# Performance work log

Hardware: AMD Instinct MI355X
Metric: run time of the kernel (lower is better)

## Reference

```python
import jax, jax.numpy as jnp
import numpy as np

NUM_EXPERTS = 8
TOP_K = 2
HIDDEN = 1024
INTER = 4096
B, S = 4, 2048


def setup_inputs() -> dict:
    key = jax.random.key(0)
    ks = jax.random.split(key, 5)
    scale_h = 1.0 / np.sqrt(HIDDEN)
    scale_f = 1.0 / np.sqrt(INTER)
    return {
        "hidden_states": jax.random.normal(ks[0], (B, S, HIDDEN), dtype=jnp.float32),
        "router_w": jax.random.normal(ks[1], (HIDDEN, NUM_EXPERTS), dtype=jnp.float32) * scale_h,
        "gate_w": jax.random.normal(ks[2], (NUM_EXPERTS, HIDDEN, INTER), dtype=jnp.float32) * scale_h,
        "up_w": jax.random.normal(ks[3], (NUM_EXPERTS, HIDDEN, INTER), dtype=jnp.float32) * scale_h,
        "down_w": jax.random.normal(ks[4], (NUM_EXPERTS, INTER, HIDDEN), dtype=jnp.float32) * scale_f,
    }


def reference(hidden_states, router_w, gate_w, up_w, down_w):
    # hidden_states: [B, S, D]
    Bsz, Sl, D = hidden_states.shape
    E = gate_w.shape[0]

    router_logits = jnp.einsum("bsd,de->bse", hidden_states, router_w)
    router_probs = jax.nn.softmax(router_logits, axis=-1)          # [B,S,E]
    expert_weights, expert_indices = jax.lax.top_k(router_probs, TOP_K)  # [B,S,K]
    expert_weights = expert_weights / jnp.sum(expert_weights, axis=-1, keepdims=True)

    # load-balance loss: usage_e = count(idx==e)/num_tokens (sums to K)
    num_tokens = Bsz * Sl
    one_hot = jax.nn.one_hot(expert_indices, E, dtype=router_probs.dtype)  # [B,S,K,E]
    expert_usage = jnp.sum(one_hot, axis=(0, 1, 2)) / num_tokens           # [E]
    mean_routing_prob = jnp.mean(router_probs, axis=(0, 1))                # [E]
    load_balance_loss = jnp.sum(expert_usage * mean_routing_prob) * E

    # combine weight per token per expert: [B,S,E]
    combine_w = jnp.einsum("bsk,bske->bse", expert_weights, one_hot)

    output = jnp.zeros_like(hidden_states)
    for e in range(E):  # small fixed expert count
        gate = jax.nn.silu(jnp.einsum("bsd,df->bsf", hidden_states, gate_w[e]))
        up = jnp.einsum("bsd,df->bsf", hidden_states, up_w[e])
        expert_out = jnp.einsum("bsf,fd->bsd", gate * up, down_w[e])
        output = output + combine_w[..., e, None] * expert_out

    return output, load_balance_loss
```

## Files before the change

kernel.cpp:

```cpp
#include <hip/hip_runtime.h>
#include <stdint.h>

#define T_TOK 8192
#define D_HID 1024
#define F_INT 4096
#define NEXP 8
#define NT2 (T_TOK*2)
#define BMR 256
#define NTIL 72
#define CBANKS 64

typedef __attribute__((ext_vector_type(4))) float f32x4;
typedef __attribute__((ext_vector_type(8))) __bf16 bf16x8;
typedef unsigned short u16;

__device__ __forceinline__ unsigned short f2bf(float x) {
  unsigned int u = __float_as_uint(x);
  u = u + 0x7FFFu + ((u >> 16) & 1u);
  return (unsigned short)(u >> 16);
}
__device__ __forceinline__ float bf2f(u16 b) {
  return __uint_as_float(((unsigned)b) << 16);
}
__device__ __forceinline__ void gload_lds16(const void* g, void* l) {
  __builtin_amdgcn_global_load_lds(
      (const __attribute__((address_space(1))) unsigned int*)g,
      (__attribute__((address_space(3))) unsigned int*)l, 16, 0, 0);
}
__device__ __forceinline__ void wait_vm8() {
  asm volatile("s_waitcnt vmcnt(8)" ::: "memory");
  __builtin_amdgcn_sched_barrier(0);
}
__device__ __forceinline__ void wait_vm0() {
  asm volatile("s_waitcnt vmcnt(0)" ::: "memory");
  __builtin_amdgcn_sched_barrier(0);
}
__device__ __forceinline__ void wait_lgkm0() {
  asm volatile("s_waitcnt lgkmcnt(0)" ::: "memory");
  __builtin_amdgcn_sched_barrier(0);
}
__device__ __forceinline__ int tswz(int x) { return (x & 7) * 9 + (x >> 3); }

#define MFMA(a,b,c) __builtin_amdgcn_mfma_f32_16x16x32_bf16((a),(b),(c),0,0,0)

__global__ __launch_bounds__(256) void k_cvt(const float* __restrict__ in,
                                             u16* __restrict__ out, long n) {
  long i = ((long)blockIdx.x * 256 + threadIdx.x) * 4;
  long stride = (long)gridDim.x * 1024;
  for (; i < n; i += stride) {
    float4 v = *(const float4*)(in + i);
    union { u16 s[4]; uint2 v2; } o;
    o.s[0] = f2bf(v.x); o.s[1] = f2bf(v.y); o.s[2] = f2bf(v.z); o.s[3] = f2bf(v.w);
    *(uint2*)(out + i) = o.v2;
  }
}

__global__ __launch_bounds__(256) void k_cvt_t(const float* __restrict__ in,
                                               u16* __restrict__ out,
                                               int R, int C) {
  const size_t mat = (size_t)R * C;
  const float* ip = in + (size_t)blockIdx.z * mat;
  u16* op = out + (size_t)blockIdx.z * mat;
  int c0 = blockIdx.x * 64, r0 = blockIdx.y * 64;
  __shared__ u16 T[64][68];
  int t = threadIdx.x;
#pragma unroll
  for (int p = 0; p < 4; p++) {
    int r = p * 16 + (t >> 4);
    int c = (t & 15) * 4;
    float4 v = *(const float4*)(ip + (size_t)(r0 + r) * C + (c0 + c));
    union { u16 s[4]; uint2 q; } o;
    o.s[0] = f2bf(v.x); o.s[1] = f2bf(v.y); o.s[2] = f2bf(v.z); o.s[3] = f2bf(v.w);
    *(uint2*)&T[r][c] = o.q;
  }
  __syncthreads();
  int f = t >> 2, seg = (t & 3) * 16;
  __align__(16) u16 buf[16];
#pragma unroll
  for (int j = 0; j < 16; j++) buf[j] = T[seg + j][f];
  *(uint4*)(op + (size_t)(c0 + f) * R + r0 + seg) = *(uint4*)&buf[0];
  *(uint4*)(op + (size_t)(c0 + f) * R + r0 + seg + 8) = *(uint4*)&buf[8];
}

__global__ __launch_bounds__(256) void k_router(const float* __restrict__ h,
                                                const float* __restrict__ rw,
                                                int* __restrict__ cntB,
                                                float* __restrict__ psumB,
                                                int* __restrict__ topk_e,
                                                float* __restrict__ topk_w) {
  int t = blockIdx.x * 4 + (threadIdx.x >> 6);
  int l = threadIdx.x & 63;
  const float* hr = h + (size_t)t * D_HID;
  double acc[NEXP];
#pragma unroll
  for (int e = 0; e < NEXP; e++) acc[e] = 0.0;
  for (int i = l; i < D_HID; i += 64) {
    double x = (double)hr[i];
    const float4* r4 = (const float4*)(rw + (size_t)i * NEXP);
    float4 a = r4[0], b = r4[1];
    acc[0] += x * a.x; acc[1] += x * a.y; acc[2] += x * a.z; acc[3] += x * a.w;
    acc[4] += x * b.x; acc[5] += x * b.y; acc[6] += x * b.z; acc[7] += x * b.w;
  }
#pragma unroll
  for (int m = 32; m >= 1; m >>= 1) {
#pragma unroll
    for (int e = 0; e < NEXP; e++) acc[e] += __shfl_xor(acc[e], m, 64);
  }
  if (l == 0) {
    double mx = acc[0];
#pragma unroll
    for (int e = 1; e < NEXP; e++) mx = fmax(mx, acc[e]);
    double p[NEXP], s = 0.0;
#pragma unroll
    for (int e = 0; e < NEXP; e++) { p[e] = exp(acc[e] - mx); s += p[e]; }
    int i0 = 0;
#pragma unroll
    for (int e = 1; e < NEXP; e++) if (p[e] > p[i0]) i0 = e;
    int i1 = (i0 == 0) ? 1 : 0;
#pragma unroll
    for (int e = 0; e < NEXP; e++) if (e != i0 && p[e] > p[i1]) i1 = e;
    double w0 = p[i0] / (p[i0] + p[i1]);
    topk_e[t] = i0 | (i1 << 8);
    topk_w[2 * t] = (float)w0;
    topk_w[2 * t + 1] = (float)(1.0 - w0);
    int bank = t & (CBANKS - 1);
    atomicAdd(&cntB[i0 * CBANKS + bank], 1);
    atomicAdd(&cntB[i1 * CBANKS + bank], 1);
    float inv = (float)(1.0 / s);
#pragma unroll
    for (int e = 0; e < NEXP; e++) atomicAdd(&psumB[e * CBANKS + bank], (float)p[e] * inv);
  }
}

__global__ void k_scan(const int* __restrict__ cntB, const float* __restrict__ psumB,
                       int* __restrict__ offs, int4* __restrict__ tiles,
                       int* __restrict__ meta, float* __restrict__ loss_out,
                       int* __restrict__ cnt2) {
  if (threadIdx.x != 0 || blockIdx.x != 0) return;
  int off = 0, tc = 0;
  double loss = 0.0;
  for (int e = 0; e < NEXP; e++) {
    int c = 0; float ps = 0.f;
    for (int b = 0; b < CBANKS; b++) { c += cntB[e * CBANKS + b]; ps += psumB[e * CBANKS + b]; }
    loss += ((double)c / (double)T_TOK) * ((double)ps / (double)T_TOK);
    offs[e] = off;
    int nt = (c + BMR - 1) / BMR;
    for (int j = 0; j < nt; j++) {
      int rem = c - j * BMR;
      tiles[tc] = make_int4(e, off + j * BMR, rem < BMR ? rem : BMR, 0);
      tc++;
    }
    off += c;
    cnt2[e] = 0;
  }
  offs[NEXP] = off;
  meta[0] = tc;
  loss_out[0] = (float)(loss * (double)NEXP);
}

__global__ __launch_bounds__(256) void k_scatter(const int* __restrict__ topk_e,
                                                 const float* __restrict__ topk_w,
                                                 const int* __restrict__ offs,
                                                 int* __restrict__ cnt2,
                                                 int* __restrict__ rowtok,
                                                 float* __restrict__ roww) {
  int t = blockIdx.x * 256 + threadIdx.x;
  if (t >= T_TOK) return;
  int ee = topk_e[t];
#pragma unroll
  for (int k = 0; k < 2; k++) {
    int e = (ee >> (8 * k)) & 255;
    int pos = offs[e] + atomicAdd(&cnt2[e], 1);
    rowtok[pos] = t;
    roww[pos] = topk_w[2 * t + k];
  }
}

template <int MODE>
__global__ __launch_bounds__(512, 2) void k_mm8(
    const u16* __restrict__ Asrc, const u16* __restrict__ Bsrc,
    const int4* __restrict__ tiles, const int* __restrict__ meta,
    const int* __restrict__ rowtok, const float* __restrict__ roww,
    u16* __restrict__ G, float* __restrict__ out,
    int fcb, int FC, int KLEN) {
  int bx = tswz(blockIdx.x);
  if (bx >= meta[0]) return;
  int4 td = tiles[bx];
  int eid = td.x, row0 = td.y, nrows = td.z;
  int by = blockIdx.y;
  int kz_byte = (int)blockIdx.z * KLEN * 2;

  __shared__ __align__(16) u16 lds[2][2][BMR][64];

  int tid = threadIdx.x;
  int l = tid & 63, wid = tid >> 6;
  int wr = wid >> 2, wc = wid & 3;

  int rr0 = wid * 8 + (l >> 3);
  int sw = ((l & 7) ^ (rr0 & 7)) << 4;
  const char* pA[4]; const char* pB[4];
#pragma unroll
  for (int j = 0; j < 4; j++) {
    int rr = j * 64 + rr0;
    if constexpr (MODE < 2) {
      int tok = rowtok[row0 + ((rr < nrows) ? rr : 0)];
      pA[j] = (const char*)Asrc + (size_t)tok * (D_HID * 2) + sw;
      int brow = fcb + by * 256 + rr;
      pB[j] = (const char*)Bsrc + ((size_t)eid * F_INT + brow) * (D_HID * 2) + sw;
    } else {
      pA[j] = (const char*)Asrc + (size_t)(row0 + rr) * (FC * 2) + kz_byte + sw;
      int brow = by * 256 + rr;
      pB[j] = (const char*)Bsrc + ((size_t)eid * D_HID + brow) * (F_INT * 2) + kz_byte + sw;
    }
  }

  int ch0 = (((l >> 4) + 0) ^ (l & 7)) << 4;
  int ch1 = (((l >> 4) + 4) ^ (l & 7)) << 4;
  int offA = (wr * 128 + (l & 15)) * 128;
  int offB = 32768 + (wc * 64 + (l & 15)) * 128;
  const char* base = (const char*)&lds[0][0][0][0];
#define LDA(b,m,s) (*(const bf16x8*)(base + (b)*65536 + offA + (m)*2048 + ((s)?ch1:ch0)))
#define LDB(b,n,s) (*(const bf16x8*)(base + (b)*65536 + offB + (n)*2048 + ((s)?ch1:ch0)))

  f32x4 acc[8][4];
#pragma unroll
  for (int m = 0; m < 8; m++)
#pragma unroll
    for (int n = 0; n < 4; n++) acc[m][n] = f32x4{0.f, 0.f, 0.f, 0.f};

  auto STAGE = [&](int b, int mat, const char* const* p, int kt) {
#pragma unroll
    for (int j = 0; j < 4; j++)
      gload_lds16(p[j] + (size_t)kt * 128, &lds[b][mat][j * 64 + wid * 8][0]);
  };

  auto TILE = [&](int b, int kts, bool dostage, int vm) {
    bf16x8 fa[4][2], fb[4][2];
#pragma unroll
    for (int m = 0; m < 4; m++) { fa[m][0] = LDA(b, m, 0); fa[m][1] = LDA(b, m, 1); }
#pragma unroll
    for (int n = 0; n < 2; n++) { fb[n][0] = LDB(b, n, 0); fb[n][1] = LDB(b, n, 1); }
    __builtin_amdgcn_s_barrier();
    wait_lgkm0();
    __builtin_amdgcn_s_setprio(1);
#pragma unroll
    for (int m = 0; m < 4; m++)
#pragma unroll
      for (int n = 0; n < 2; n++) {
        acc[m][n] = MFMA(fa[m][0], fb[n][0], acc[m][n]);
        acc[m][n] = MFMA(fa[m][1], fb[n][1], acc[m][n]);
      }
    __builtin_amdgcn_s_setprio(0);
    __builtin_amdgcn_s_barrier();
#pragma unroll
    for (int n = 2; n < 4; n++) { fb[n][0] = LDB(b, n, 0); fb[n][1] = LDB(b, n, 1); }
    __builtin_amdgcn_s_barrier();
    wait_lgkm0();
    __builtin_amdgcn_s_setprio(1);
#pragma unroll
    for (int m = 0; m < 4; m++)
#pragma unroll
      for (int n = 2; n < 4; n++) {
        acc[m][n] = MFMA(fa[m][0], fb[n][0], acc[m][n]);
        acc[m][n] = MFMA(fa[m][1], fb[n][1], acc[m][n]);
      }
    __builtin_amdgcn_s_setprio(0);
    __builtin_amdgcn_s_barrier();
#pragma unroll
    for (int m = 0; m < 4; m++) { fa[m][0] = LDA(b, 4 + m, 0); fa[m][1] = LDA(b, 4 + m, 1); }
    if (dostage) STAGE(b, 1, pB, kts);
    __builtin_amdgcn_s_barrier();
    wait_lgkm0();
    __builtin_amdgcn_s_setprio(1);
#pragma unroll
    for (int m = 0; m < 4; m++)
#pragma unroll
      for (int n = 0; n < 2; n++) {
        acc[4 + m][n] = MFMA(fa[m][0], fb[n][0], acc[4 + m][n]);
        acc[4 + m][n] = MFMA(fa[m][1], fb[n][1], acc[4 + m][n]);
      }
    __builtin_amdgcn_s_setprio(0);
    __builtin_amdgcn_s_barrier();
    if (dostage) STAGE(b, 0, pA, kts);
    if (vm == 8) wait_vm8();
    else if (vm == 0) wait_vm0();
    __builtin_amdgcn_s_barrier();
    __builtin_amdgcn_s_setprio(1);
#pragma unroll
    for (int m = 0; m < 4; m++)
#pragma unroll
      for (int n = 2; n < 4; n++) {
        acc[4 + m][n] = MFMA(fa[m][0], fb[n][0], acc[4 + m][n]);
        acc[4 + m][n] = MFMA(fa[m][1], fb[n][1], acc[4 + m][n]);
      }
    __builtin_amdgcn_s_setprio(0);
    __builtin_amdgcn_s_barrier();
  };

  int NT = KLEN / 64;
  STAGE(0, 1, pB, 0); STAGE(0, 0, pA, 0);
  STAGE(1, 1, pB, 1); STAGE(1, 0, pA, 1);
  wait_vm8();
  __builtin_amdgcn_s_barrier();

  int NIT = NT / 2;
  for (int it = 0; it < NIT - 1; ++it) {
    TILE(0, 2 * it + 2, true, 8);
    TILE(1, 2 * it + 3, true, 8);
  }
  TILE(0, 0, false, 0);
  TILE(1, 0, false, -1);

  int lr = (l >> 4) * 4, lc = l & 15;
#pragma unroll
  for (int m = 0; m < 8; m++) {
    int rbase = wr * 128 + m * 16 + lr;
#pragma unroll
    for (int j = 0; j < 4; j++) {
      int r = rbase + j;
      if (r < nrows) {
        if constexpr (MODE == 0) {
          size_t gb = (size_t)(row0 + r) * FC + by * 256 + wc * 64 + lc;
#pragma unroll
          for (int n = 0; n < 4; n++) G[gb + n * 16] = f2bf(acc[m][n][j]);
        } else if constexpr (MODE == 1) {
          size_t gb = (size_t)(row0 + r) * FC + by * 256 + wc * 64 + lc;
#pragma unroll
          for (int n = 0; n < 4; n++) {
            float g = bf2f(G[gb + n * 16]);
            float sv = g / (1.0f + __expf(-g));
            G[gb + n * 16] = f2bf(sv * acc[m][n][j]);
          }
        } else {
          float w = roww[row0 + r];
          int tok = rowtok[row0 + r];
          size_t ob = (size_t)tok * D_HID + by * 256 + wc * 64 + lc;
#pragma unroll
          for (int n = 0; n < 4; n++) atomicAdd(&out[ob + n * 16], acc[m][n][j] * w);
        }
      }
    }
  }
#undef LDA
#undef LDB
}

extern "C" void kernel_launch(void* const* d_in, const int* in_sizes, int n_in,
                              void* d_out, int out_size, void* d_ws, size_t ws_size,
                              hipStream_t stream) {
  (void)in_sizes; (void)n_in;
  const float* h  = (const float*)d_in[0];
  const float* rw = (const float*)d_in[1];
  const float* gw = (const float*)d_in[2];
  const float* uw = (const float*)d_in[3];
  const float* dw = (const float*)d_in[4];
  float* out = (float*)d_out;

  char* base = (char*)d_ws;
  size_t off = 0;
  auto alloc = [&](size_t b) -> char* {
    char* r = base + off;
    off += (b + 255) & ~(size_t)255;
    return r;
  };

  u16*   hb     = (u16*)alloc((size_t)T_TOK * D_HID * 2);
  int*   cntB   = (int*)alloc(NEXP * CBANKS * 4);
  float* psumB  = (float*)alloc(NEXP * CBANKS * 4);
  int*   offs   = (int*)alloc((NEXP + 1) * 4);
  int*   cnt2   = (int*)alloc(NEXP * 4);
  int*   meta   = (int*)alloc(64);
  int4*  tiles  = (int4*)alloc(NTIL * sizeof(int4));
  int*   topk_e = (int*)alloc(T_TOK * 4);
  float* topk_w = (float*)alloc((size_t)T_TOK * 2 * 4);
  int*   rowtok = (int*)alloc(NT2 * 4);
  float* roww   = (float*)alloc(NT2 * 4);

  size_t zbytes = (size_t)((char*)topk_e - (char*)cntB);

  const size_t GROWS = NT2 + (size_t)BMR * NEXP;
  const size_t EDF = (size_t)NEXP * D_HID * F_INT;
  size_t avail = (ws_size > off) ? ws_size - off : 0;
  auto need = [&](int nc) -> size_t {
    return 3 * EDF * 2 + GROWS * (size_t)(F_INT / nc) * 2 + 65536;
  };
  int nchunk = 4;
  if      (avail >= need(1)) nchunk = 1;
  else if (avail >= need(2)) nchunk = 2;
  u16* gT = (u16*)alloc(EDF * 2);
  u16* uT = (u16*)alloc(EDF * 2);
  u16* dT = (u16*)alloc(EDF * 2);
  int FC = F_INT / nchunk;
  u16* G = (u16*)alloc(GROWS * (size_t)FC * 2);

  hipMemsetAsync(d_out, 0, (size_t)out_size * 4, stream);
  hipMemsetAsync(cntB, 0, zbytes, stream);

  k_cvt<<<2048, 256, 0, stream>>>(h, hb, (long)T_TOK * D_HID);
  {
    dim3 gt(F_INT / 64, D_HID / 64, NEXP);
    k_cvt_t<<<gt, 256, 0, stream>>>(gw, gT, D_HID, F_INT);
    k_cvt_t<<<gt, 256, 0, stream>>>(uw, uT, D_HID, F_INT);
    dim3 dt(D_HID / 64, F_INT / 64, NEXP);
    k_cvt_t<<<dt, 256, 0, stream>>>(dw, dT, F_INT, D_HID);
  }
  k_router<<<T_TOK / 4, 256, 0, stream>>>(h, rw, cntB, psumB, topk_e, topk_w);
  k_scan<<<1, 64, 0, stream>>>(cntB, psumB, offs, tiles, meta, out + (out_size - 1), cnt2);
  k_scatter<<<T_TOK / 256, 256, 0, stream>>>(topk_e, topk_w, offs, cnt2, rowtok, roww);

  for (int c = 0; c < nchunk; c++) {
    int fcb = c * FC;
    dim3 g1(NTIL, FC / 256, 1);
    dim3 g2(NTIL, D_HID / 256, 2);
    k_mm8<0><<<g1, 512, 0, stream>>>(hb, gT, tiles, meta, rowtok, roww, G, out,
                                     fcb, FC, D_HID);
    k_mm8<1><<<g1, 512, 0, stream>>>(hb, uT, tiles, meta, rowtok, roww, G, out,
                                     fcb, FC, D_HID);
    k_mm8<2><<<g2, 512, 0, stream>>>(G, dT, tiles, meta, rowtok, roww, G, out,
                                     fcb, FC, FC / 2);
  }
}
```

Measured before the change: 976.7 us.

## Fuse gate and up projections into one GEMM and simplify pipeline

Merges the gate and up GEMMs into one kernel. Each block loads 128 gate rows and 128 up rows of weights into the same B tile and applies SiLU(gate)*up in the epilogue. This removes one launch per chunk, one read of the gathered activations, and the bf16 round trip of the gate result through G. It also replaces the hand-interleaved 8-phase MFMA/barrier schedule with a simpler double-buffer loop that waits for all loads each step, which may expose more memory latency.

```diff
diff --git a/kernel.cpp b/kernel.cpp
--- a/kernel.cpp
+++ b/kernel.cpp
@@ -27,16 +27,8 @@
       (const __attribute__((address_space(1))) unsigned int*)g,
       (__attribute__((address_space(3))) unsigned int*)l, 16, 0, 0);
 }
-__device__ __forceinline__ void wait_vm8() {
-  asm volatile("s_waitcnt vmcnt(8)" ::: "memory");
-  __builtin_amdgcn_sched_barrier(0);
-}
 __device__ __forceinline__ void wait_vm0() {
   asm volatile("s_waitcnt vmcnt(0)" ::: "memory");
-  __builtin_amdgcn_sched_barrier(0);
-}
-__device__ __forceinline__ void wait_lgkm0() {
-  asm volatile("s_waitcnt lgkmcnt(0)" ::: "memory");
   __builtin_amdgcn_sched_barrier(0);
 }
 __device__ __forceinline__ int tswz(int x) { return (x & 7) * 9 + (x >> 3); }
@@ -177,8 +169,9 @@
 }
 
 template <int MODE>
-__global__ __launch_bounds__(512, 2) void k_mm8(
+__global__ __launch_bounds__(512, 2) void k_mm2(
     const u16* __restrict__ Asrc, const u16* __restrict__ Bsrc,
+    const u16* __restrict__ Bsrc2,
     const int4* __restrict__ tiles, const int* __restrict__ meta,
     const int* __restrict__ rowtok, const float* __restrict__ roww,
     u16* __restrict__ G, float* __restrict__ out,
@@ -188,12 +181,11 @@
   int4 td = tiles[bx];
   int eid = td.x, row0 = td.y, nrows = td.z;
   int by = blockIdx.y;
-  int kz_byte = (int)blockIdx.z * KLEN * 2;
+  size_t kz_byte = (size_t)blockIdx.z * KLEN * 2;
 
   __shared__ __align__(16) u16 lds[2][2][BMR][64];
 
-  int tid = threadIdx.x;
-  int l = tid & 63, wid = tid >> 6;
+  int tid = threadIdx.x, l = tid & 63, wid = tid >> 6;
   int wr = wid >> 2, wc = wid & 3;
 
   int rr0 = wid * 8 + (l >> 3);
@@ -202,11 +194,12 @@
 #pragma unroll
   for (int j = 0; j < 4; j++) {
     int rr = j * 64 + rr0;
-    if constexpr (MODE < 2) {
+    if constexpr (MODE == 0) {
       int tok = rowtok[row0 + ((rr < nrows) ? rr : 0)];
       pA[j] = (const char*)Asrc + (size_t)tok * (D_HID * 2) + sw;
-      int brow = fcb + by * 256 + rr;
-      pB[j] = (const char*)Bsrc + ((size_t)eid * F_INT + brow) * (D_HID * 2) + sw;
+      const u16* wsrc = (j < 2) ? Bsrc : Bsrc2;
+      int frow = fcb + by * 128 + (rr & 127);
+      pB[j] = (const char*)wsrc + ((size_t)eid * F_INT + frow) * (D_HID * 2) + sw;
     } else {
       pA[j] = (const char*)Asrc + (size_t)(row0 + rr) * (FC * 2) + kz_byte + sw;
       int brow = by * 256 + rr;
@@ -216,11 +209,18 @@
 
   int ch0 = (((l >> 4) + 0) ^ (l & 7)) << 4;
   int ch1 = (((l >> 4) + 4) ^ (l & 7)) << 4;
-  int offA = (wr * 128 + (l & 15)) * 128;
-  int offB = 32768 + (wc * 64 + (l & 15)) * 128;
-  const char* base = (const char*)&lds[0][0][0][0];
-#define LDA(b,m,s) (*(const bf16x8*)(base + (b)*65536 + offA + (m)*2048 + ((s)?ch1:ch0)))
-#define LDB(b,n,s) (*(const bf16x8*)(base + (b)*65536 + offB + (n)*2048 + ((s)?ch1:ch0)))
+  int arow = (wr * 128 + (l & 15)) * 128;
+  int brow[4];
+#pragma unroll
+  for (int n = 0; n < 4; n++) {
+    int r;
+    if constexpr (MODE == 0)
+      r = (n < 2) ? (wc * 32 + n * 16 + (l & 15)) : (128 + wc * 32 + (n - 2) * 16 + (l & 15));
+    else
+      r = wc * 64 + n * 16 + (l & 15);
+    brow[n] = 32768 + r * 128;
+  }
+  const char* lbase = (const char*)&lds[0][0][0][0];
 
   f32x4 acc[8][4];
 #pragma unroll
@@ -228,108 +228,69 @@
 #pragma unroll
     for (int n = 0; n < 4; n++) acc[m][n] = f32x4{0.f, 0.f, 0.f, 0.f};
 
-  auto STAGE = [&](int b, int mat, const char* const* p, int kt) {
-#pragma unroll
-    for (int j = 0; j < 4; j++)
-      gload_lds16(p[j] + (size_t)kt * 128, &lds[b][mat][j * 64 + wid * 8][0]);
+  auto STAGE = [&](int b, int kt) {
+#pragma unroll
+    for (int j = 0; j < 4; j++) {
+      gload_lds16(pA[j] + (size_t)kt * 128, &lds[b][0][j * 64 + wid * 8][0]);
+      gload_lds16(pB[j] + (size_t)kt * 128, &lds[b][1][j * 64 + wid * 8][0]);
+    }
   };
 
-  auto TILE = [&](int b, int kts, bool dostage, int vm) {
-    bf16x8 fa[4][2], fb[4][2];
-#pragma unroll
-    for (int m = 0; m < 4; m++) { fa[m][0] = LDA(b, m, 0); fa[m][1] = LDA(b, m, 1); }
-#pragma unroll
-    for (int n = 0; n < 2; n++) { fb[n][0] = LDB(b, n, 0); fb[n][1] = LDB(b, n, 1); }
+  auto COMPUTE = [&](int bufoff) {
+    __builtin_amdgcn_s_setprio(1);
+#pragma unroll
+    for (int ks = 0; ks < 2; ks++) {
+      int ch = ks ? ch1 : ch0;
+      bf16x8 fb0 = *(const bf16x8*)(lbase + bufoff + brow[0] + ch);
+      bf16x8 fb1 = *(const bf16x8*)(lbase + bufoff + brow[1] + ch);
+      bf16x8 fb2 = *(const bf16x8*)(lbase + bufoff + brow[2] + ch);
+      bf16x8 fb3 = *(const bf16x8*)(lbase + bufoff + brow[3] + ch);
+#pragma unroll
+      for (int m = 0; m < 8; m++) {
+        bf16x8 fa = *(const bf16x8*)(lbase + bufoff + arow + m * 2048 + ch);
+        acc[m][0] = MFMA(fa, fb0, acc[m][0]);
+        acc[m][1] = MFMA(fa, fb1, acc[m][1]);
+        acc[m][2] = MFMA(fa, fb2, acc[m][2]);
+        acc[m][3] = MFMA(fa, fb3, acc[m][3]);
+      }
+    }
+    __builtin_amdgcn_s_setprio(0);
+  };
+
+  int NT = KLEN / 64;
+  STAGE(0, 0);
+  wait_vm0();
+  __builtin_amdgcn_s_barrier();
+  for (int it = 0; it < NT / 2; ++it) {
+    int t0 = 2 * it;
+    STAGE(1, t0 + 1);
+    COMPUTE(0);
+    wait_vm0();
     __builtin_amdgcn_s_barrier();
-    wait_lgkm0();
-    __builtin_amdgcn_s_setprio(1);
-#pragma unroll
-    for (int m = 0; m < 4; m++)
-#pragma unroll
-      for (int n = 0; n < 2; n++) {
-        acc[m][n] = MFMA(fa[m][0], fb[n][0], acc[m][n]);
-        acc[m][n] = MFMA(fa[m][1], fb[n][1], acc[m][n]);
-      }
-    __builtin_amdgcn_s_setprio(0);
-    __builtin_amdgcn_s_barrier();
-#pragma unroll
-    for (int n = 2; n < 4; n++) { fb[n][0] = LDB(b, n, 0); fb[n][1] = LDB(b, n, 1); }
-    __builtin_amdgcn_s_barrier();
-    wait_lgkm0();
-    __builtin_amdgcn_s_setprio(1);
-#pragma unroll
-    for (int m = 0; m < 4; m++)
-#pragma unroll
-      for (int n = 2; n < 4; n++) {
-        acc[m][n] = MFMA(fa[m][0], fb[n][0], acc[m][n]);
-        acc[m][n] = MFMA(fa[m][1], fb[n][1], acc[m][n]);
-      }
-    __builtin_amdgcn_s_setprio(0);
-    __builtin_amdgcn_s_barrier();
-#pragma unroll
-    for (int m = 0; m < 4; m++) { fa[m][0] = LDA(b, 4 + m, 0); fa[m][1] = LDA(b, 4 + m, 1); }
-    if (dostage) STAGE(b, 1, pB, kts);
-    __builtin_amdgcn_s_barrier();
-    wait_lgkm0();
-    __builtin_amdgcn_s_setprio(1);
-#pragma unroll
-    for (int m = 0; m < 4; m++)
-#pragma unroll
-      for (int n = 0; n < 2; n++) {
-        acc[4 + m][n] = MFMA(fa[m][0], fb[n][0], acc[4 + m][n]);
-        acc[4 + m][n] = MFMA(fa[m][1], fb[n][1], acc[4 + m][n]);
-      }
-    __builtin_amdgcn_s_setprio(0);
-    __builtin_amdgcn_s_barrier();
-    if (dostage) STAGE(b, 0, pA, kts);
-    if (vm == 8) wait_vm8();
-    else if (vm == 0) wait_vm0();
-    __builtin_amdgcn_s_barrier();
-    __builtin_amdgcn_s_setprio(1);
-#pragma unroll
-    for (int m = 0; m < 4; m++)
-#pragma unroll
-      for (int n = 2; n < 4; n++) {
-        acc[4 + m][n] = MFMA(fa[m][0], fb[n][0], acc[4 + m][n]);
-        acc[4 + m][n] = MFMA(fa[m][1], fb[n][1], acc[4 + m][n]);
-      }
-    __builtin_amdgcn_s_setprio(0);
-    __builtin_amdgcn_s_barrier();
-  };
-
-  int NT = KLEN / 64;
-  STAGE(0, 1, pB, 0); STAGE(0, 0, pA, 0);
-  STAGE(1, 1, pB, 1); STAGE(1, 0, pA, 1);
-  wait_vm8();
-  __builtin_amdgcn_s_barrier();
-
-  int NIT = NT / 2;
-  for (int it = 0; it < NIT - 1; ++it) {
-    TILE(0, 2 * it + 2, true, 8);
-    TILE(1, 2 * it + 3, true, 8);
-  }
-  TILE(0, 0, false, 0);
-  TILE(1, 0, false, -1);
+    if (t0 + 2 < NT) {
+      STAGE(0, t0 + 2);
+      COMPUTE(65536);
+      wait_vm0();
+      __builtin_amdgcn_s_barrier();
+    } else {
+      COMPUTE(65536);
+    }
+  }
 
   int lr = (l >> 4) * 4, lc = l & 15;
 #pragma unroll
   for (int m = 0; m < 8; m++) {
-    int rbase = wr * 128 + m * 16 + lr;
 #pragma unroll
     for (int j = 0; j < 4; j++) {
-      int r = rbase + j;
+      int r = wr * 128 + m * 16 + lr + j;
       if (r < nrows) {
         if constexpr (MODE == 0) {
-          size_t gb = (size_t)(row0 + r) * FC + by * 256 + wc * 64 + lc;
-#pragma unroll
-          for (int n = 0; n < 4; n++) G[gb + n * 16] = f2bf(acc[m][n][j]);
-        } else if constexpr (MODE == 1) {
-          size_t gb = (size_t)(row0 + r) * FC + by * 256 + wc * 64 + lc;
-#pragma unroll
-          for (int n = 0; n < 4; n++) {
-            float g = bf2f(G[gb + n * 16]);
+          size_t gb = (size_t)(row0 + r) * FC + by * 128 + wc * 32 + lc;
+#pragma unroll
+          for (int n = 0; n < 2; n++) {
+            float g = acc[m][n][j], u = acc[m][n + 2][j];
             float sv = g / (1.0f + __expf(-g));
-            G[gb + n * 16] = f2bf(sv * acc[m][n][j]);
+            G[gb + n * 16] = f2bf(sv * u);
           }
         } else {
           float w = roww[row0 + r];
@@ -341,8 +302,6 @@
       }
     }
   }
-#undef LDA
-#undef LDB
 }
 
 extern "C" void kernel_launch(void* const* d_in, const int* in_sizes, int n_in,
@@ -410,13 +369,11 @@
 
   for (int c = 0; c < nchunk; c++) {
     int fcb = c * FC;
-    dim3 g1(NTIL, FC / 256, 1);
+    dim3 g1(NTIL, FC / 128, 1);
     dim3 g2(NTIL, D_HID / 256, 2);
-    k_mm8<0><<<g1, 512, 0, stream>>>(hb, gT, tiles, meta, rowtok, roww, G, out,
+    k_mm2<0><<<g1, 512, 0, stream>>>(hb, gT, uT, tiles, meta, rowtok, roww, G, out,
                                      fcb, FC, D_HID);
-    k_mm8<1><<<g1, 512, 0, stream>>>(hb, uT, tiles, meta, rowtok, roww, G, out,
-                                     fcb, FC, D_HID);
-    k_mm8<2><<<g2, 512, 0, stream>>>(G, dT, tiles, meta, rowtok, roww, G, out,
+    k_mm2<2><<<g2, 512, 0, stream>>>(G, dT, dT, tiles, meta, rowtok, roww, G, out,
                                      fcb, FC, FC / 2);
   }
 }
```

Result: slower. 3.373 ms (+245.3%).

## Fuse gate and up projections into one GEMM with SiLU epilogue

Applied to the files above, without the earlier changes.

The gate and up GEMMs are merged into one kernel. Each block now loads 128 gate-weight rows and 128 up-weight rows into its B tile and applies SiLU(gate)*up directly from the accumulators. This drops one kernel launch per chunk, the bf16 round-trip of the gate result through G, and the second gather of the A rows. The cost is twice as many blocks in the first grid, each producing half as many output columns, and an extra B-offset table held in registers.

```diff
diff --git a/kernel.cpp b/kernel.cpp
--- a/kernel.cpp
+++ b/kernel.cpp
@@ -18,9 +18,6 @@
   unsigned int u = __float_as_uint(x);
   u = u + 0x7FFFu + ((u >> 16) & 1u);
   return (unsigned short)(u >> 16);
-}
-__device__ __forceinline__ float bf2f(u16 b) {
-  return __uint_as_float(((unsigned)b) << 16);
 }
 __device__ __forceinline__ void gload_lds16(const void* g, void* l) {
   __builtin_amdgcn_global_load_lds(
@@ -179,6 +176,7 @@
 template <int MODE>
 __global__ __launch_bounds__(512, 2) void k_mm8(
     const u16* __restrict__ Asrc, const u16* __restrict__ Bsrc,
+    const u16* __restrict__ Bsrc2,
     const int4* __restrict__ tiles, const int* __restrict__ meta,
     const int* __restrict__ rowtok, const float* __restrict__ roww,
     u16* __restrict__ G, float* __restrict__ out,
@@ -188,7 +186,7 @@
   int4 td = tiles[bx];
   int eid = td.x, row0 = td.y, nrows = td.z;
   int by = blockIdx.y;
-  int kz_byte = (int)blockIdx.z * KLEN * 2;
+  size_t kz_byte = (size_t)blockIdx.z * KLEN * 2;
 
   __shared__ __align__(16) u16 lds[2][2][BMR][64];
 
@@ -202,11 +200,12 @@
 #pragma unroll
   for (int j = 0; j < 4; j++) {
     int rr = j * 64 + rr0;
-    if constexpr (MODE < 2) {
+    if constexpr (MODE == 0) {
       int tok = rowtok[row0 + ((rr < nrows) ? rr : 0)];
       pA[j] = (const char*)Asrc + (size_t)tok * (D_HID * 2) + sw;
-      int brow = fcb + by * 256 + rr;
-      pB[j] = (const char*)Bsrc + ((size_t)eid * F_INT + brow) * (D_HID * 2) + sw;
+      const u16* wsrc = (j < 2) ? Bsrc : Bsrc2;
+      int frow = fcb + by * 128 + (rr & 127);
+      pB[j] = (const char*)wsrc + ((size_t)eid * F_INT + frow) * (D_HID * 2) + sw;
     } else {
       pA[j] = (const char*)Asrc + (size_t)(row0 + rr) * (FC * 2) + kz_byte + sw;
       int brow = by * 256 + rr;
@@ -217,10 +216,19 @@
   int ch0 = (((l >> 4) + 0) ^ (l & 7)) << 4;
   int ch1 = (((l >> 4) + 4) ^ (l & 7)) << 4;
   int offA = (wr * 128 + (l & 15)) * 128;
-  int offB = 32768 + (wc * 64 + (l & 15)) * 128;
+  int offBn[4];
+#pragma unroll
+  for (int n = 0; n < 4; n++) {
+    int r;
+    if constexpr (MODE == 0)
+      r = (n < 2) ? (wc * 32 + n * 16) : (128 + wc * 32 + (n - 2) * 16);
+    else
+      r = wc * 64 + n * 16;
+    offBn[n] = 32768 + (r + (l & 15)) * 128;
+  }
   const char* base = (const char*)&lds[0][0][0][0];
 #define LDA(b,m,s) (*(const bf16x8*)(base + (b)*65536 + offA + (m)*2048 + ((s)?ch1:ch0)))
-#define LDB(b,n,s) (*(const bf16x8*)(base + (b)*65536 + offB + (n)*2048 + ((s)?ch1:ch0)))
+#define LDB(b,n,s) (*(const bf16x8*)(base + (b)*65536 + offBn[n] + ((s)?ch1:ch0)))
 
   f32x4 acc[8][4];
 #pragma unroll
@@ -320,16 +328,12 @@
       int r = rbase + j;
       if (r < nrows) {
         if constexpr (MODE == 0) {
-          size_t gb = (size_t)(row0 + r) * FC + by * 256 + wc * 64 + lc;
-#pragma unroll
-          for (int n = 0; n < 4; n++) G[gb + n * 16] = f2bf(acc[m][n][j]);
-        } else if constexpr (MODE == 1) {
-          size_t gb = (size_t)(row0 + r) * FC + by * 256 + wc * 64 + lc;
-#pragma unroll
-          for (int n = 0; n < 4; n++) {
-            float g = bf2f(G[gb + n * 16]);
+          size_t gb = (size_t)(row0 + r) * FC + by * 128 + wc * 32 + lc;
+#pragma unroll
+          for (int n = 0; n < 2; n++) {
+            float g = acc[m][n][j], u = acc[m][n + 2][j];
             float sv = g / (1.0f + __expf(-g));
-            G[gb + n * 16] = f2bf(sv * acc[m][n][j]);
+            G[gb + n * 16] = f2bf(sv * u);
           }
         } else {
           float w = roww[row0 + r];
@@ -410,13 +414,11 @@
 
   for (int c = 0; c < nchunk; c++) {
     int fcb = c * FC;
-    dim3 g1(NTIL, FC / 256, 1);
+    dim3 g1(NTIL, FC / 128, 1);
     dim3 g2(NTIL, D_HID / 256, 2);
-    k_mm8<0><<<g1, 512, 0, stream>>>(hb, gT, tiles, meta, rowtok, roww, G, out,
+    k_mm8<0><<<g1, 512, 0, stream>>>(hb, gT, uT, tiles, meta, rowtok, roww, G, out,
                                      fcb, FC, D_HID);
-    k_mm8<1><<<g1, 512, 0, stream>>>(hb, uT, tiles, meta, rowtok, roww, G, out,
-                                     fcb, FC, D_HID);
-    k_mm8<2><<<g2, 512, 0, stream>>>(G, dT, tiles, meta, rowtok, roww, G, out,
+    k_mm8<2><<<g2, 512, 0, stream>>>(G, dT, dT, tiles, meta, rowtok, roww, G, out,
                                      fcb, FC, FC / 2);
   }
 }
```

Measured after the change: 880.4 us. 9.9% less time.
